# Kernel optimization log

Hardware: AMD Instinct MI355X
Metric: run time of the kernel (lower is better)

Reference implementation:

```python
import jax, jax.numpy as jnp
import numpy as np

N_NODES = 10000
N_EDGES = 320000
D_FEAT = 128


def setup_inputs() -> dict:
    key = jax.random.key(0)
    k1, k2, k3 = jax.random.split(key, 3)
    node_states = jax.random.normal(k1, (N_NODES, D_FEAT), dtype=jnp.float32)
    edge_sources = jax.random.randint(k2, (N_EDGES,), 0, N_NODES, dtype=jnp.int32).astype(jnp.int64)
    edge_targets = jax.random.randint(k3, (N_EDGES,), 0, N_NODES, dtype=jnp.int32).astype(jnp.int64)
    return {"node_states": node_states, "edge_sources": edge_sources, "edge_targets": edge_targets}


def reference(node_states, edge_sources, edge_targets):
    # Original torch code computes one_hot(edge_sources) @ node_states, which is
    # mathematically an index-gather of node rows per edge. We implement the
    # equivalent gather directly (same math, no O(E*N) wasted GEMM work).
    msg_from_source = jnp.take(node_states, edge_sources, axis=0)  # [E, D]
    msg_from_target = jnp.take(node_states, edge_targets, axis=0)  # [E, D]
    node_msgs = jnp.concatenate([msg_from_source, msg_from_target], axis=-1)  # [E, 2D]
    return node_msgs
```

## Files before the change

### kernel.cpp

```cpp
#include <hip/hip_runtime.h>
#include <hip/hip_bf16.h>


typedef float v4f __attribute__((ext_vector_type(4)));

__global__ __launch_bounds__(256) void NodePropagator_75110388073048_kernel(
    const v4f* __restrict__ ns,
    const int* __restrict__ src32,
    const int* __restrict__ tgt32,
    v4f* __restrict__ out,
    int nEdges)
{
    int tid  = blockIdx.x * blockDim.x + threadIdx.x;
    int e    = tid >> 6;
    if (e >= nEdges) return;
    int lane = tid & 63;
    int half = lane >> 5;
    int c    = lane & 31;

    bool is_i64 = (src32[1] == 0) & (src32[3] == 0) &
                  (src32[5] == 0) & (src32[7] == 0);

    const int* idxp = half ? tgt32 : src32;
    int row;
    if (is_i64) {
        row = (int)((const long long*)idxp)[e];
    } else {
        row = idxp[e];
    }

    v4f v = ns[row * 32 + c];
    __builtin_nontemporal_store(v, &out[e * 64 + lane]);
}

extern "C" void kernel_launch(void* const* d_in, const int* in_sizes, int n_in,
                              void* d_out, int out_size, void* d_ws, size_t ws_size,
                              hipStream_t stream) {
    const v4f* ns  = (const v4f*)d_in[0];
    const int* src = (const int*)d_in[1];
    const int* tgt = (const int*)d_in[2];
    v4f*       out = (v4f*)d_out;

    int nEdges = in_sizes[1];
    long long totalThreads = (long long)nEdges * 64;
    int block = 256;
    int grid  = (int)((totalThreads + block - 1) / block);

    NodePropagator_75110388073048_kernel<<<grid, block, 0, stream>>>(
        ns, src, tgt, out, nEdges);
}
```

Baseline: 364.6 us.

## Use persistent waves with double-buffered multi-edge gather batches

Each wave now processes groups of 8 edges in a grid-stride loop over a fixed 2048-block grid. It issues the index loads and row gathers for the next group before storing the current one. The aim is more loads in flight per wave, hiding gather latency and reducing per-edge block scheduling overhead. In exchange, each thread uses more registers and fewer waves are resident than in the one-edge-per-wave launch.

```diff
diff --git a/kernel.cpp b/kernel.cpp
--- a/kernel.cpp
+++ b/kernel.cpp
@@ -1,36 +1,82 @@
 #include <hip/hip_runtime.h>
-#include <hip/hip_bf16.h>
 
 
 typedef float v4f __attribute__((ext_vector_type(4)));
+
+#define EPW 8
 
 __global__ __launch_bounds__(256) void NodePropagator_75110388073048_kernel(
     const v4f* __restrict__ ns,
     const int* __restrict__ src32,
     const int* __restrict__ tgt32,
     v4f* __restrict__ out,
-    int nEdges)
+    int nEdges, int nGroups, int totalWaves)
 {
     int tid  = blockIdx.x * blockDim.x + threadIdx.x;
-    int e    = tid >> 6;
-    if (e >= nEdges) return;
+    int wid  = tid >> 6;
     int lane = tid & 63;
     int half = lane >> 5;
     int c    = lane & 31;
 
     bool is_i64 = (src32[1] == 0) & (src32[3] == 0) &
                   (src32[5] == 0) & (src32[7] == 0);
+    int stride = is_i64 ? 2 : 1;
 
     const int* idxp = half ? tgt32 : src32;
-    int row;
-    if (is_i64) {
-        row = (int)((const long long*)idxp)[e];
-    } else {
-        row = idxp[e];
+
+#define LOADIDX(g, rows)                                        \
+    {                                                           \
+        int base_ = (g) * EPW;                                  \
+        _Pragma("unroll")                                       \
+        for (int k = 0; k < EPW; ++k) {                         \
+            int e_ = base_ + k;                                 \
+            if (e_ >= nEdges) e_ = nEdges - 1;                  \
+            rows[k] = idxp[e_ * stride];                        \
+        }                                                       \
     }
 
-    v4f v = ns[row * 32 + c];
-    __builtin_nontemporal_store(v, &out[e * 64 + lane]);
+#define GATHER(rows, v)                                         \
+    {                                                           \
+        _Pragma("unroll")                                       \
+        for (int k = 0; k < EPW; ++k)                           \
+            v[k] = ns[rows[k] * 32 + c];                        \
+    }
+
+#define STORE(v, g)                                             \
+    {                                                           \
+        int base_ = (g) * EPW;                                  \
+        _Pragma("unroll")                                       \
+        for (int k = 0; k < EPW; ++k) {                         \
+            int e_ = base_ + k;                                 \
+            if (e_ < nEdges)                                    \
+                __builtin_nontemporal_store(v[k],               \
+                    &out[e_ * 64 + lane]);                      \
+        }                                                       \
+    }
+
+    int gA = wid;
+    if (gA >= nGroups) return;
+
+    int rA[EPW]; v4f vA[EPW];
+    int rB[EPW]; v4f vB[EPW];
+
+    LOADIDX(gA, rA);
+    GATHER(rA, vA);
+
+    while (true) {
+        int gB = gA + totalWaves;
+        bool hB = gB < nGroups;
+        if (hB) { LOADIDX(gB, rB); GATHER(rB, vB); }
+        STORE(vA, gA);
+        if (!hB) return;
+
+        int gC = gB + totalWaves;
+        bool hC = gC < nGroups;
+        if (hC) { LOADIDX(gC, rA); GATHER(rA, vA); }
+        STORE(vB, gB);
+        if (!hC) return;
+        gA = gC;
+    }
 }
 
 extern "C" void kernel_launch(void* const* d_in, const int* in_sizes, int n_in,
@@ -41,11 +87,17 @@
     const int* tgt = (const int*)d_in[2];
     v4f*       out = (v4f*)d_out;
 
-    int nEdges = in_sizes[1];
-    long long totalThreads = (long long)nEdges * 64;
+    int nEdges  = in_sizes[1];
+    int nGroups = (nEdges + EPW - 1) / EPW;
+
     int block = 256;
-    int grid  = (int)((totalThreads + block - 1) / block);
+    int grid  = 2048;
+    int totalWaves = grid * (block / 64);
+    if (totalWaves > nGroups) {
+        totalWaves = nGroups;
+        grid = (totalWaves + (block / 64) - 1) / (block / 64);
+    }
 
     NodePropagator_75110388073048_kernel<<<grid, block, 0, stream>>>(
-        ns, src, tgt, out, nEdges);
+        ns, src, tgt, out, nEdges, nGroups, totalWaves);
 }
```

Result: faster. 342.1 us (-6.2%).
